# Performance work log

Measured on AMD Instinct MI355X. Metric: run time of the kernel, lower is better.

Reference implementation:

```python
import jax, jax.numpy as jnp
import numpy as np

H = 12  # max_heads

def setup_inputs() -> dict:
    key = jax.random.key(0)
    ks = jax.random.split(key, 5)
    B, N, E = 8, 1024, 768
    return {
        "x": jax.random.normal(ks[0], (B, N, E), dtype=jnp.float32),
        "w_qkv": jax.random.normal(ks[1], (3 * E, E), dtype=jnp.float32) * 0.02,
        "b_qkv": jax.random.normal(ks[2], (3 * E,), dtype=jnp.float32) * 0.02,
        "w_proj": jax.random.normal(ks[3], (E, E), dtype=jnp.float32) * 0.02,
        "b_proj": jax.random.normal(ks[4], (E,), dtype=jnp.float32) * 0.02,
        "active_heads": 8,
    }

def reference(x, w_qkv, b_qkv, w_proj, b_proj, active_heads):
    B, N, E = x.shape
    D = E // H
    scale = D ** -0.5
    # qkv projection: [B,N,3E] -> [3,B,H,N,D]
    qkv = (x @ w_qkv.T + b_qkv).reshape(B, N, 3, H, D)
    qkv = jnp.transpose(qkv, (2, 0, 3, 1, 4))
    q, k, v = qkv[0], qkv[1], qkv[2]
    # head mask from active_heads (static int)
    head_mask = (jnp.arange(H) < active_heads).astype(x.dtype)
    m = head_mask[None, :, None, None]
    q = q * m
    k = k * m
    v = v * m
    attn = jax.nn.softmax(jnp.einsum("bhqd,bhkd->bhqk", q, k) * scale, axis=-1)
    out = jnp.einsum("bhqk,bhkd->bhqd", attn, v)
    out = jnp.transpose(out, (0, 2, 1, 3)).reshape(B, N, E)
    channel_mask = jnp.repeat(head_mask, D)  # [E]
    out = out * channel_mask[None, None, :]
    return out @ w_proj.T + b_proj
```

## Files before the change

### kernel.cpp

```cpp
#include <hip/hip_runtime.h>
#include <hip/hip_fp16.h>

#define NH 12
#define BSZ 8
#define NSEQ 1024
#define EDIM 768
#define DH 64

typedef _Float16 f16;
typedef f16 half8 __attribute__((ext_vector_type(8)));
typedef f16 half4 __attribute__((ext_vector_type(4)));
typedef float f32x4 __attribute__((ext_vector_type(4)));
typedef unsigned int u32;
typedef u32 u32x2 __attribute__((ext_vector_type(2)));

static __device__ __forceinline__ void gload16(const void* g, void* l) {
    __builtin_amdgcn_global_load_lds((const __attribute__((address_space(1))) u32*)g,
                                     (__attribute__((address_space(3))) u32*)l, 16, 0, 0);
}
static __device__ __forceinline__ u32 pkrtz(float a, float b) {
    auto h = __builtin_amdgcn_cvt_pkrtz(a, b);
    return __builtin_bit_cast(u32, h);
}
#define MFMA16(a, b, c) __builtin_amdgcn_mfma_f32_16x16x32_f16((a), (b), (c), 0, 0, 0)

__global__ void cvt_all_kernel(const float* __restrict__ x, const float* __restrict__ wq,
                               const float* __restrict__ wp, f16* __restrict__ dst) {
    const int NX = BSZ * NSEQ * EDIM;
    const int NWQ = 3 * EDIM * EDIM;
    int i = (blockIdx.x * blockDim.x + threadIdx.x) * 4;
    const float* s;
    int j;
    if (i < NX) { s = x; j = i; }
    else if (i < NX + NWQ) { s = wq; j = i - NX; }
    else { s = wp; j = i - NX - NWQ; }
    float4 v = *(const float4*)(s + j);
    half4 o = { (f16)v.x, (f16)v.y, (f16)v.z, (f16)v.w };
    *(half4*)(dst + i) = o;
}

template<int MODE>
__global__ __launch_bounds__(256) void gemm_kernel(
    const f16* __restrict__ A, const f16* __restrict__ Wt, const float* __restrict__ bias,
    f16* __restrict__ qbuf, f16* __restrict__ kbuf, f16* __restrict__ vbuf,
    float* __restrict__ outp, const int* __restrict__ activep, int Kd, int NCd)
{
    __shared__ __align__(16) f16 Ah[2][2][4][64][8];
    __shared__ __align__(16) f16 Bh[2][2][4][64][8];

    constexpr int K = EDIM;
    constexpr int NKT = K / 32;
    constexpr int NB = (MODE == 0) ? 18 : 6;

    const int lin = blockIdx.x;
    const int xcd = lin & 7, pos = lin >> 3;
    const int bx = pos % NB;
    const int my = xcd + (pos / NB) * 8;
    const int c0 = bx * 128;
    const int m0 = my * 128;
    const int ah = *activep;
    if (MODE == 0) {
        if (((c0 % EDIM) >> 6) >= ah) return;
    }
    const int nkt = (MODE == 1) ? (2 * ah) : NKT;
    const int tid = threadIdx.x;
    const int lane = tid & 63;
    const int wid  = tid >> 6;
    const int wr = wid >> 1;
    const int wc = wid & 1;
    const int r16 = lane & 15, rg = lane >> 4;

    f32x4 acc[4][4];
#pragma unroll
    for (int i = 0; i < 4; ++i)
#pragma unroll
        for (int j = 0; j < 4; ++j)
            acc[i][j] = f32x4{0.f, 0.f, 0.f, 0.f};

    const int s0 = 2 * wid, s1 = 2 * wid + 1;
    const f16* gA0 = A  + (size_t)(m0 + (s0 >> 2) * 64 + (s0 & 3) * 16 + r16) * K + rg * 8;
    const f16* gA1 = A  + (size_t)(m0 + (s1 >> 2) * 64 + (s1 & 3) * 16 + r16) * K + rg * 8;
    const f16* gB0 = Wt + (size_t)(c0 + (s0 >> 2) * 64 + (s0 & 3) * 16 + r16) * K + rg * 8;
    const f16* gB1 = Wt + (size_t)(c0 + (s1 >> 2) * 64 + (s1 & 3) * 16 + r16) * K + rg * 8;

    auto stage = [&](int buf, int kt) {
        gload16(gA0 + kt * 32, &Ah[buf][s0 >> 2][s0 & 3][0][0]);
        gload16(gA1 + kt * 32, &Ah[buf][s1 >> 2][s1 & 3][0][0]);
        gload16(gB0 + kt * 32, &Bh[buf][s0 >> 2][s0 & 3][0][0]);
        gload16(gB1 + kt * 32, &Bh[buf][s1 >> 2][s1 & 3][0][0]);
    };

    if (nkt > 0) stage(0, 0);
    if (nkt > 1) stage(1, 1);
    asm volatile("s_waitcnt vmcnt(4)" ::: "memory");
    __builtin_amdgcn_s_barrier();
    __builtin_amdgcn_sched_barrier(0);

#pragma unroll 1
    for (int kt = 0; kt < nkt; ++kt) {
        const int cur = kt & 1;
        half8 af[4], bf[4];
#pragma unroll
        for (int f = 0; f < 4; ++f) {
            af[f] = *(const half8*)&Ah[cur][wr][f][lane][0];
            bf[f] = *(const half8*)&Bh[cur][wc][f][lane][0];
        }
        asm volatile("s_waitcnt lgkmcnt(0)" ::: "memory");
        __builtin_amdgcn_sched_barrier(0);
        __builtin_amdgcn_s_barrier();
        __builtin_amdgcn_sched_barrier(0);
        if (kt + 2 < nkt) stage(cur, kt + 2);
        __builtin_amdgcn_sched_barrier(0);
        __builtin_amdgcn_s_setprio(1);
#pragma unroll
        for (int fm = 0; fm < 4; ++fm)
#pragma unroll
            for (int fn = 0; fn < 4; ++fn)
                acc[fm][fn] = MFMA16(af[fm], bf[fn], acc[fm][fn]);
        __builtin_amdgcn_s_setprio(0);
        if (kt + 1 < nkt) {
            if (kt + 2 < nkt) asm volatile("s_waitcnt vmcnt(4)" ::: "memory");
            else              asm volatile("s_waitcnt vmcnt(0)" ::: "memory");
            __builtin_amdgcn_s_barrier();
            __builtin_amdgcn_sched_barrier(0);
        }
    }

#pragma unroll
    for (int fn = 0; fn < 4; ++fn) {
        const int c = c0 + wc * 64 + fn * 16 + r16;
        const float bv = bias[c];
        const bool colActive = (MODE == 1) || (((c % EDIM) >> 6) < ah);
#pragma unroll
        for (int fm = 0; fm < 4; ++fm) {
            const int mbase = m0 + wr * 64 + fm * 16 + rg * 4;
#pragma unroll
            for (int r = 0; r < 4; ++r) {
                const float val = acc[fm][fn][r] + bv;
                const int m = mbase + r;
                if (MODE == 1) {
                    outp[(size_t)m * EDIM + c] = val;
                } else if (colActive) {
                    const int s  = c / EDIM;
                    const int cc = c % EDIM;
                    const int hh = cc >> 6, d = cc & 63;
                    const int bb = m >> 10, n = m & 1023;
                    f16* dst = (s == 0) ? qbuf : ((s == 1) ? kbuf : vbuf);
                    dst[(((size_t)bb * NH + hh) * NSEQ + n) * DH + d] = (f16)val;
                }
            }
        }
    }
}

__global__ __launch_bounds__(256) void vtrans_kernel(const f16* __restrict__ vbuf,
                                                     f16* __restrict__ vtb,
                                                     const int* __restrict__ activep) {
    const int b = blockIdx.z, h = blockIdx.y;
    if (h >= *activep) return;
    const int n0 = blockIdx.x * 64;
    __shared__ __align__(16) f16 T[64][72];
    const f16* src = vbuf + (((size_t)b * NH + h) * NSEQ + n0) * DH;
    f16* dst = vtb + ((size_t)b * NH + h) * DH * NSEQ;
    const int t = threadIdx.x;
    const int rn = t >> 2, rc = t & 3;
    *(half8*)&T[rn][rc * 16]     = *(const half8*)&src[(size_t)rn * DH + rc * 16];
    *(half8*)&T[rn][rc * 16 + 8] = *(const half8*)&src[(size_t)rn * DH + rc * 16 + 8];
    __syncthreads();
    const int d = t >> 2, nc = (t & 3) * 16;
    half8 o0, o1;
#pragma unroll
    for (int j = 0; j < 8; ++j) {
        o0[j] = T[nc + j][d];
        o1[j] = T[nc + 8 + j][d];
    }
    *(half8*)&dst[(size_t)d * NSEQ + n0 + nc]     = o0;
    *(half8*)&dst[(size_t)d * NSEQ + n0 + nc + 8] = o1;
}

__global__ __launch_bounds__(512) void attn_kernel(
    const f16* __restrict__ qbuf, const f16* __restrict__ kbuf, const f16* __restrict__ vtb,
    f16* __restrict__ ctx, const int* __restrict__ activep)
{
    __shared__ __align__(16) f16 Kh[2][64][64];
    __shared__ __align__(16) f16 Vh[2][64][64];
    __shared__ __align__(16) f16 Ph[8][16][64];

    const int b = blockIdx.z, h = blockIdx.y;
    const int q0 = blockIdx.x * 128;
    const int tid = threadIdx.x, lane = tid & 63, wid = tid >> 6;

    if (h >= *activep) return;

    const size_t hb = (((size_t)b * NH + h) * NSEQ) * DH;
    const f16* Q  = qbuf + hb;
    const char* Kp = (const char*)(kbuf + hb);
    const char* Vp = (const char*)(vtb + hb);

    const int ql = lane & 15;
    const int g  = lane >> 4;
    const int q7 = ql & 7;

    half8 qb0, qb1;
    {
        const f16 qsc = (f16)0.18033688f;
        const f16* qp = Q + (size_t)(q0 + wid * 16 + ql) * DH + g * 8;
        qb0 = *(const half8*)qp        * qsc;
        qb1 = *(const half8*)(qp + 32) * qsc;
    }
    const half8 ones = { (f16)1, (f16)1, (f16)1, (f16)1, (f16)1, (f16)1, (f16)1, (f16)1 };

    const int srow8 = lane >> 3;
    const int schk  = (lane & 7) ^ srow8;
    const int qh4   = wid & 3;

    auto stage = [&](int buf, int kt) {
        if (wid < 4) {
            const char* kb = Kp + (size_t)kt * 8192;
#pragma unroll
            for (int i = 0; i < 2; ++i) {
                const int r = qh4 * 16 + i * 8 + srow8;
                gload16(kb + (size_t)r * 128 + schk * 16, &Kh[buf][qh4 * 16 + i * 8][0]);
            }
        } else {
#pragma unroll
            for (int i = 0; i < 2; ++i) {
                const int r = qh4 * 16 + i * 8 + srow8;
                gload16(Vp + (size_t)r * (NSEQ * 2) + (size_t)kt * 128 + schk * 16,
                        &Vh[buf][qh4 * 16 + i * 8][0]);
            }
        }
    };

    f32x4 oacc[4];
#pragma unroll
    for (int i = 0; i < 4; ++i) oacc[i] = f32x4{0.f, 0.f, 0.f, 0.f};
    f32x4 lacc = f32x4{0.f, 0.f, 0.f, 0.f};
    float mr = -INFINITY;

    char* prow = (char*)&Ph[wid][ql][0];

    stage(0, 0);
    const int NT = NSEQ / 64;
    for (int kt = 0; kt < NT; ++kt) {
        const int cur = kt & 1;
        __syncthreads();
        if (kt + 1 < NT) stage(cur ^ 1, kt + 1);

        f32x4 st[4];
        __builtin_amdgcn_s_setprio(1);
#pragma unroll
        for (int s = 0; s < 4; ++s) {
            f32x4 t = f32x4{0.f, 0.f, 0.f, 0.f};
            t = MFMA16(*(const half8*)((const char*)&Kh[cur][16 * s + ql][0] + ((g ^ q7) << 4)),       qb0, t);
            t = MFMA16(*(const half8*)((const char*)&Kh[cur][16 * s + ql][0] + (((4 | g) ^ q7) << 4)), qb1, t);
            st[s] = t;
        }
        __builtin_amdgcn_s_setprio(0);

        float a0 = fmaxf(fmaxf(st[0][0], st[0][1]), st[0][2]);
        float a1 = fmaxf(fmaxf(st[0][3], st[1][0]), st[1][1]);
        float a2 = fmaxf(fmaxf(st[1][2], st[1][3]), st[2][0]);
        float a3 = fmaxf(fmaxf(st[2][1], st[2][2]), st[2][3]);
        float a4 = fmaxf(fmaxf(st[3][0], st[3][1]), st[3][2]);
        float pmax = fmaxf(fmaxf(fmaxf(a0, a1), fmaxf(a2, a3)), fmaxf(a4, st[3][3]));
        pmax = fmaxf(pmax, __shfl_xor(pmax, 16));
        pmax = fmaxf(pmax, __shfl_xor(pmax, 32));

        const float mnew = fmaxf(mr, pmax);
        const float sc = exp2f(mr - mnew);
#pragma unroll
        for (int s = 0; s < 4; ++s)
#pragma unroll
            for (int r = 0; r < 4; ++r)
                st[s][r] = exp2f(st[s][r] - mnew);
        mr = mnew;

#pragma unroll
        for (int r = 0; r < 4; ++r) {
            const float scr = __shfl(sc, (g << 2) | r);
            oacc[0][r] *= scr; oacc[1][r] *= scr; oacc[2][r] *= scr; oacc[3][r] *= scr;
            lacc[r] *= scr;
        }

#pragma unroll
        for (int s = 0; s < 4; ++s) {
            u32x2 w = { pkrtz(st[s][0], st[s][1]), pkrtz(st[s][2], st[s][3]) };
            *(u32x2*)(prow + ((32 * s + 8 * g) ^ (q7 << 4))) = w;
        }
        const half8 pa0 = *(const half8*)(prow + ((16 * g) ^ (q7 << 4)));
        const half8 pa1 = *(const half8*)(prow + ((64 + 16 * g) ^ (q7 << 4)));

        __builtin_amdgcn_s_setprio(1);
        lacc = MFMA16(pa0, ones, lacc);
        lacc = MFMA16(pa1, ones, lacc);
#pragma unroll
        for (int db = 0; db < 4; ++db) {
            oacc[db] = MFMA16(pa0, *(const half8*)((const char*)&Vh[cur][16 * db + ql][0] + ((g ^ q7) << 4)),       oacc[db]);
            oacc[db] = MFMA16(pa1, *(const half8*)((const char*)&Vh[cur][16 * db + ql][0] + (((4 | g) ^ q7) << 4)), oacc[db]);
        }
        __builtin_amdgcn_s_setprio(0);
    }

#pragma unroll
    for (int r = 0; r < 4; ++r) {
        const float li = 1.0f / lacc[r];
        const int n = q0 + wid * 16 + (g << 2) + r;
#pragma unroll
        for (int db = 0; db < 4; ++db)
            ctx[((size_t)b * NSEQ + n) * EDIM + h * DH + db * 16 + ql] = (f16)(oacc[db][r] * li);
    }
}

extern "C" void kernel_launch(void* const* d_in, const int* in_sizes, int n_in,
                              void* d_out, int out_size, void* d_ws, size_t ws_size,
                              hipStream_t stream) {
    const float* x      = (const float*)d_in[0];
    const float* w_qkv  = (const float*)d_in[1];
    const float* b_qkv  = (const float*)d_in[2];
    const float* w_proj = (const float*)d_in[3];
    const float* b_proj = (const float*)d_in[4];
    const int*   active = (const int*)d_in[5];
    float* out = (float*)d_out;

    char* ws = (char*)d_ws;
    const size_t n_x  = (size_t)BSZ * NSEQ * EDIM;
    const size_t n_wq = (size_t)3 * EDIM * EDIM;
    const size_t n_wp = (size_t)EDIM * EDIM;
    const size_t n_hd = (size_t)BSZ * NH * NSEQ * DH;

    f16* xh   = (f16*)ws;
    f16* wqh  = xh + n_x;
    f16* wph  = wqh + n_wq;
    f16* qh   = wph + n_wp;
    f16* kh   = qh + n_hd;
    f16* vh   = kh + n_hd;
    f16* ctxh = vh + n_hd;
    f16* vtb  = xh;

    const size_t n_cvt = n_x + n_wq + n_wp;
    cvt_all_kernel<<<(int)(n_cvt / 4 / 256), 256, 0, stream>>>(x, w_qkv, w_proj, xh);

    gemm_kernel<0><<<dim3(64 * 18), 256, 0, stream>>>(
        xh, wqh, b_qkv, qh, kh, vh, nullptr, active, EDIM, 3 * EDIM);

    vtrans_kernel<<<dim3(NSEQ / 64, NH, BSZ), 256, 0, stream>>>(vh, vtb, active);

    attn_kernel<<<dim3(NSEQ / 128, NH, BSZ), 512, 0, stream>>>(qh, kh, vtb, ctxh, active);

    gemm_kernel<1><<<dim3(64 * 6), 256, 0, stream>>>(
        ctxh, wph, b_proj, nullptr, nullptr, nullptr, out, active, EDIM, EDIM);
}
```

Measured before the change: 118.0 us.

## Fuse fp32-to-fp16 conversion of x into the QKV GEMM tile loads

```diff
diff --git a/kernel.cpp b/kernel.cpp
--- a/kernel.cpp
+++ b/kernel.cpp
@@ -24,16 +24,14 @@
 }
 #define MFMA16(a, b, c) __builtin_amdgcn_mfma_f32_16x16x32_f16((a), (b), (c), 0, 0, 0)
 
-__global__ void cvt_all_kernel(const float* __restrict__ x, const float* __restrict__ wq,
-                               const float* __restrict__ wp, f16* __restrict__ dst) {
-    const int NX = BSZ * NSEQ * EDIM;
+__global__ void cvt_w_kernel(const float* __restrict__ wq, const float* __restrict__ wp,
+                             f16* __restrict__ dst) {
     const int NWQ = 3 * EDIM * EDIM;
     int i = (blockIdx.x * blockDim.x + threadIdx.x) * 4;
     const float* s;
     int j;
-    if (i < NX) { s = x; j = i; }
-    else if (i < NX + NWQ) { s = wq; j = i - NX; }
-    else { s = wp; j = i - NX - NWQ; }
+    if (i < NWQ) { s = wq; j = i; }
+    else { s = wp; j = i - NWQ; }
     float4 v = *(const float4*)(s + j);
     half4 o = { (f16)v.x, (f16)v.y, (f16)v.z, (f16)v.w };
     *(half4*)(dst + i) = o;
@@ -41,16 +39,17 @@
 
 template<int MODE>
 __global__ __launch_bounds__(256) void gemm_kernel(
-    const f16* __restrict__ A, const f16* __restrict__ Wt, const float* __restrict__ bias,
+    const void* __restrict__ Avp, const f16* __restrict__ Wt, const float* __restrict__ bias,
     f16* __restrict__ qbuf, f16* __restrict__ kbuf, f16* __restrict__ vbuf,
     float* __restrict__ outp, const int* __restrict__ activep, int Kd, int NCd)
 {
-    __shared__ __align__(16) f16 Ah[2][2][4][64][8];
-    __shared__ __align__(16) f16 Bh[2][2][4][64][8];
-
     constexpr int K = EDIM;
     constexpr int NKT = K / 32;
     constexpr int NB = (MODE == 0) ? 18 : 6;
+    constexpr int ASLOTS = (MODE == 0) ? 16 : 8;
+
+    __shared__ __align__(16) char Ah[2 * ASLOTS * 1024];
+    __shared__ __align__(16) f16 Bh[2][2][4][64][8];
 
     const int lin = blockIdx.x;
     const int xcd = lin & 7, pos = lin >> 3;
@@ -78,21 +77,37 @@
             acc[i][j] = f32x4{0.f, 0.f, 0.f, 0.f};
 
     const int s0 = 2 * wid, s1 = 2 * wid + 1;
-    const f16* gA0 = A  + (size_t)(m0 + (s0 >> 2) * 64 + (s0 & 3) * 16 + r16) * K + rg * 8;
-    const f16* gA1 = A  + (size_t)(m0 + (s1 >> 2) * 64 + (s1 & 3) * 16 + r16) * K + rg * 8;
+    const int rA0 = m0 + (s0 >> 2) * 64 + (s0 & 3) * 16 + r16;
+    const int rA1 = m0 + (s1 >> 2) * 64 + (s1 & 3) * 16 + r16;
     const f16* gB0 = Wt + (size_t)(c0 + (s0 >> 2) * 64 + (s0 & 3) * 16 + r16) * K + rg * 8;
     const f16* gB1 = Wt + (size_t)(c0 + (s1 >> 2) * 64 + (s1 & 3) * 16 + r16) * K + rg * 8;
 
     auto stage = [&](int buf, int kt) {
-        gload16(gA0 + kt * 32, &Ah[buf][s0 >> 2][s0 & 3][0][0]);
-        gload16(gA1 + kt * 32, &Ah[buf][s1 >> 2][s1 & 3][0][0]);
+        if constexpr (MODE == 0) {
+            const float* A32 = (const float*)Avp;
+            const float* p0 = A32 + (size_t)rA0 * K + kt * 32 + rg * 8;
+            const float* p1 = A32 + (size_t)rA1 * K + kt * 32 + rg * 8;
+            char* d = Ah + (size_t)buf * ASLOTS * 1024;
+            gload16(p0,     d + (s0 * 2 + 0) * 1024);
+            gload16(p0 + 4, d + (s0 * 2 + 1) * 1024);
+            gload16(p1,     d + (s1 * 2 + 0) * 1024);
+            gload16(p1 + 4, d + (s1 * 2 + 1) * 1024);
+        } else {
+            const f16* A16 = (const f16*)Avp;
+            const f16* p0 = A16 + (size_t)rA0 * K + kt * 32 + rg * 8;
+            const f16* p1 = A16 + (size_t)rA1 * K + kt * 32 + rg * 8;
+            char* d = Ah + (size_t)buf * ASLOTS * 1024;
+            gload16(p0, d + s0 * 1024);
+            gload16(p1, d + s1 * 1024);
+        }
         gload16(gB0 + kt * 32, &Bh[buf][s0 >> 2][s0 & 3][0][0]);
         gload16(gB1 + kt * 32, &Bh[buf][s1 >> 2][s1 & 3][0][0]);
     };
 
     if (nkt > 0) stage(0, 0);
     if (nkt > 1) stage(1, 1);
-    asm volatile("s_waitcnt vmcnt(4)" ::: "memory");
+    if constexpr (MODE == 0) asm volatile("s_waitcnt vmcnt(6)" ::: "memory");
+    else                     asm volatile("s_waitcnt vmcnt(4)" ::: "memory");
     __builtin_amdgcn_s_barrier();
     __builtin_amdgcn_sched_barrier(0);
 
@@ -102,7 +117,17 @@
         half8 af[4], bf[4];
 #pragma unroll
         for (int f = 0; f < 4; ++f) {
-            af[f] = *(const half8*)&Ah[cur][wr][f][lane][0];
+            if constexpr (MODE == 0) {
+                const char* ab = Ah + (size_t)cur * ASLOTS * 1024
+                               + ((wr * 4 + f) * 2) * 1024 + lane * 16;
+                float4 lo = *(const float4*)ab;
+                float4 hi = *(const float4*)(ab + 1024);
+                af[f] = half8{ (f16)lo.x, (f16)lo.y, (f16)lo.z, (f16)lo.w,
+                               (f16)hi.x, (f16)hi.y, (f16)hi.z, (f16)hi.w };
+            } else {
+                af[f] = *(const half8*)(Ah + (size_t)cur * ASLOTS * 1024
+                                        + (wr * 4 + f) * 1024 + lane * 16);
+            }
             bf[f] = *(const half8*)&Bh[cur][wc][f][lane][0];
         }
         asm volatile("s_waitcnt lgkmcnt(0)" ::: "memory");
@@ -119,8 +144,12 @@
                 acc[fm][fn] = MFMA16(af[fm], bf[fn], acc[fm][fn]);
         __builtin_amdgcn_s_setprio(0);
         if (kt + 1 < nkt) {
-            if (kt + 2 < nkt) asm volatile("s_waitcnt vmcnt(4)" ::: "memory");
-            else              asm volatile("s_waitcnt vmcnt(0)" ::: "memory");
+            if (kt + 2 < nkt) {
+                if constexpr (MODE == 0) asm volatile("s_waitcnt vmcnt(6)" ::: "memory");
+                else                     asm volatile("s_waitcnt vmcnt(4)" ::: "memory");
+            } else {
+                asm volatile("s_waitcnt vmcnt(0)" ::: "memory");
+            }
             __builtin_amdgcn_s_barrier();
             __builtin_amdgcn_sched_barrier(0);
         }
@@ -324,25 +353,23 @@
     float* out = (float*)d_out;
 
     char* ws = (char*)d_ws;
-    const size_t n_x  = (size_t)BSZ * NSEQ * EDIM;
     const size_t n_wq = (size_t)3 * EDIM * EDIM;
     const size_t n_wp = (size_t)EDIM * EDIM;
     const size_t n_hd = (size_t)BSZ * NH * NSEQ * DH;
 
-    f16* xh   = (f16*)ws;
-    f16* wqh  = xh + n_x;
+    f16* wqh  = (f16*)ws;
     f16* wph  = wqh + n_wq;
     f16* qh   = wph + n_wp;
     f16* kh   = qh + n_hd;
     f16* vh   = kh + n_hd;
-    f16* ctxh = vh + n_hd;
-    f16* vtb  = xh;
-
-    const size_t n_cvt = n_x + n_wq + n_wp;
-    cvt_all_kernel<<<(int)(n_cvt / 4 / 256), 256, 0, stream>>>(x, w_qkv, w_proj, xh);
+    f16* vtb  = vh + n_hd;
+    f16* ctxh = vtb + n_hd;
+
+    const size_t n_cvt = n_wq + n_wp;
+    cvt_w_kernel<<<(int)(n_cvt / 4 / 256), 256, 0, stream>>>(w_qkv, w_proj, wqh);
 
     gemm_kernel<0><<<dim3(64 * 18), 256, 0, stream>>>(
-        xh, wqh, b_qkv, qh, kh, vh, nullptr, active, EDIM, 3 * EDIM);
+        x, wqh, b_qkv, qh, kh, vh, nullptr, active, EDIM, 3 * EDIM);
 
     vtrans_kernel<<<dim3(NSEQ / 64, NH, BSZ), 256, 0, stream>>>(vh, vtb, active);
 
```

New measurement: 129.9 us. +10.1%, slower.
